# Kernel optimization log

Measured on AMD Instinct MI355X. Metric: run time of the kernel, lower is better.

Reference implementation:

```python
import jax, jax.numpy as jnp
import numpy as np

ALPHA = 0.2  # LeakyReLU negative slope
NEG_INF = -1e9


def setup_inputs() -> dict:
    key = jax.random.key(0)
    k1, k2, k3, k4 = jax.random.split(key, 4)
    B, N, Fin, Fout = 8, 2048, 128, 64
    h = jax.random.normal(k1, (B, N, Fin), dtype=jnp.float32)
    adj_mask = jax.random.randint(k2, (B, N, N), 0, 2).astype(jnp.int32)
    # xavier_uniform-style scales
    W = jax.random.uniform(k3, (Fout, Fin), dtype=jnp.float32,
                           minval=-1.0, maxval=1.0) * np.sqrt(6.0 / (Fin + Fout))
    a = jax.random.uniform(k4, (2 * Fout,), dtype=jnp.float32,
                           minval=-1.0, maxval=1.0) * np.sqrt(6.0 / (2 * Fout + 1))
    return {"h": h, "adj_mask": adj_mask, "W": W, "a": a}


def reference(h, adj_mask, W, a):
    # Wh: [B, N, Fout]
    Wh = jnp.einsum("bnf,of->bno", h, W)
    Fout = Wh.shape[-1]
    a1, a2 = a[:Fout], a[Fout:]
    # additive decomposition of a([Wh_i || Wh_j]): e_ij = leakyrelu(s1_i + s2_j)
    s1 = Wh @ a1  # [B, N]
    s2 = Wh @ a2  # [B, N]
    e = jax.nn.leaky_relu(s1[:, :, None] + s2[:, None, :], negative_slope=ALPHA)  # [B,N,N]
    e = jnp.where(adj_mask == 0, NEG_INF, e)
    attention = jax.nn.softmax(e, axis=-1)
    # dropout is identity in eval mode / p effectively 0 for the reference
    h_prime = jnp.einsum("bij,bjo->bio", attention, Wh)
    return h_prime
```

## Files before the change

kernel.cpp:

```cpp
#include <hip/hip_runtime.h>
#include <hip/hip_fp16.h>
#include <math.h>

#define LRELU_ALPHA 0.2f
#define NEG_INF -1000000000.0f

constexpr int B_ = 8, N_ = 2048, FIN = 128, FOUT = 64;

typedef _Float16 __attribute__((ext_vector_type(8))) f16x8;
typedef float __attribute__((ext_vector_type(4))) f32x4;

__device__ __forceinline__ void gload16(const void* g, void* l) {
  __builtin_amdgcn_global_load_lds(
      (const __attribute__((address_space(1))) void*)g,
      (__attribute__((address_space(3))) void*)l, 16, 0, 0);
}

__global__ __launch_bounds__(256) void k_wh(
    const float* __restrict__ h, const float* __restrict__ W,
    const float* __restrict__ a, unsigned short* __restrict__ WhT,
    float* __restrict__ s1, float* __restrict__ s2) {
  __shared__ float Wt[128][65];
  __shared__ float hs[16][128];

  const int t = threadIdx.x;
  const int row0 = blockIdx.x * 16;

  for (int e = t; e < 64 * 128; e += 256) {
    int o = e >> 7, f = e & 127;
    Wt[f][o] = W[e];
  }
  {
    const float4* hg = (const float4*)(h + (size_t)row0 * FIN);
    for (int i4 = t; i4 < 16 * 32; i4 += 256) {
      int r = i4 >> 5, f4 = i4 & 31;
      *(float4*)&hs[r][f4 * 4] = hg[i4];
    }
  }
  __syncthreads();

  const int wave = t >> 6, lane = t & 63;
  float acc[4] = {0.f, 0.f, 0.f, 0.f};
#pragma unroll 4
  for (int f4 = 0; f4 < 32; ++f4) {
    float w0 = Wt[4 * f4 + 0][lane], w1 = Wt[4 * f4 + 1][lane];
    float w2 = Wt[4 * f4 + 2][lane], w3 = Wt[4 * f4 + 3][lane];
#pragma unroll
    for (int r = 0; r < 4; ++r) {
      float4 hv = *(const float4*)&hs[wave * 4 + r][f4 * 4];
      acc[r] += hv.x * w0 + hv.y * w1 + hv.z * w2 + hv.w * w3;
    }
  }

  const float a1v = a[lane], a2v = a[64 + lane];
  const int b = row0 / N_;
#pragma unroll
  for (int r = 0; r < 4; ++r) {
    const int row = row0 + wave * 4 + r;
    const int n = row - b * N_;
    const float v = acc[r];
    WhT[((size_t)b * 64 + lane) * N_ + n] = __half_as_ushort(__float2half(v));
    float p1 = v * a1v, p2 = v * a2v;
#pragma unroll
    for (int d = 32; d; d >>= 1) {
      p1 += __shfl_xor(p1, d, 64);
      p2 += __shfl_xor(p2, d, 64);
    }
    if (lane == 0) { s1[row] = p1; s2[row] = p2; }
  }
}

__global__ __launch_bounds__(256, 2) void k_attn(
    const unsigned short* __restrict__ WhT,
    const float* __restrict__ s1g, const float* __restrict__ s2g,
    const int* __restrict__ adj, float* __restrict__ out) {
  __shared__ __align__(16) unsigned char sA[16 * 1024];
  __shared__ __align__(16) unsigned char sB[16 * 1024];
  __shared__ float s2s[N_];
  __shared__ float lsum_lds[32];

  const int t = threadIdx.x;
  const int wave = t >> 6, lane = t & 63;
  const int m = lane & 15, q = lane >> 4;
  const int b = blockIdx.y;
  const int i0 = blockIdx.x * 32;
  const int rg = wave & 1;
  const int p0 = (wave >> 1) * 2;

  const int* adjB = adj + (size_t)b * N_ * N_;
  const unsigned short* whB = WhT + (size_t)b * 64 * N_;
  const float* s2R = s2g + b * N_;

  for (int i = t; i < N_ / 4; i += 256)
    ((float4*)s2s)[i] = ((const float4*)s2R)[i];

  const float s1r = s1g[b * N_ + i0 + rg * 16 + m];

  const unsigned char* gp[4];
  int gstr;
  if (wave < 2) {
    const size_t r = (size_t)(i0 + wave * 16 + m);
#pragma unroll
    for (int ii = 0; ii < 4; ++ii) {
      int ks = ii >> 1, hh = ii & 1;
      gp[ii] = (const unsigned char*)(adjB + r * N_ + ks * 32 + q * 8 + hh * 4);
    }
    gstr = 64 * 4;
  } else {
#pragma unroll
    for (int ii = 0; ii < 4; ++ii) {
      int g = (wave - 2) * 2 + (ii >> 1), ks = ii & 1;
      gp[ii] = (const unsigned char*)(whB + (size_t)(g * 16 + m) * N_ +
                                      ks * 32 + q * 8);
    }
    gstr = 64 * 2;
  }

#define STAGE(S, c)                                                       \
  {                                                                       \
    _Pragma("unroll") for (int ii = 0; ii < 4; ++ii)                      \
        gload16(gp[ii] + (size_t)(c) * gstr, (S) + (wave * 4 + ii) * 1024); \
  }

  f32x4 acc0 = {0.f, 0.f, 0.f, 0.f}, acc1 = acc0;
  float lsum = 0.f;

  auto consume = [&](const unsigned char* base, int c) {
#pragma unroll
    for (int ks = 0; ks < 2; ++ks) {
      int4 A0 = *(const int4*)(base + (rg * 4 + ks * 2 + 0) * 1024 + lane * 16);
      int4 A1 = *(const int4*)(base + (rg * 4 + ks * 2 + 1) * 1024 + lane * 16);
      const float* sp = &s2s[c * 64 + ks * 32 + q * 8];
      float4 sv0 = *(const float4*)sp;
      float4 sv1 = *(const float4*)(sp + 4);
      float xs[8] = {sv0.x, sv0.y, sv0.z, sv0.w, sv1.x, sv1.y, sv1.z, sv1.w};
      int avs[8] = {A0.x, A0.y, A0.z, A0.w, A1.x, A1.y, A1.z, A1.w};
      f16x8 af;
#pragma unroll
      for (int j = 0; j < 8; ++j) {
        float x = s1r + xs[j];
        float e = fmaxf(x, LRELU_ALPHA * x);
        e = avs[j] ? (e - 2.0f) : NEG_INF;
        float p = __expf(e);
        lsum += p;
        af[j] = (_Float16)p;
      }
      f16x8 b0 = *(const f16x8*)(base + (8 + (p0 + 0) * 2 + ks) * 1024 + lane * 16);
      f16x8 b1 = *(const f16x8*)(base + (8 + (p0 + 1) * 2 + ks) * 1024 + lane * 16);
      acc0 = __builtin_amdgcn_mfma_f32_16x16x32_f16(af, b0, acc0, 0, 0, 0);
      acc1 = __builtin_amdgcn_mfma_f32_16x16x32_f16(af, b1, acc1, 0, 0, 0);
    }
  };

  STAGE(sA, 0);
  __syncthreads();

  for (int cc = 0; cc < 16; ++cc) {
    const int c0 = 2 * cc, c1 = 2 * cc + 1;
    STAGE(sB, c1);
    consume(sA, c0);
    __syncthreads();
    if (c1 + 1 < 32) STAGE(sA, c1 + 1);
    consume(sB, c1);
    __syncthreads();
  }

  lsum += __shfl_xor(lsum, 16, 64);
  lsum += __shfl_xor(lsum, 32, 64);
  if (wave < 2 && lane < 16) lsum_lds[wave * 16 + lane] = lsum;
  __syncthreads();

#pragma unroll
  for (int r = 0; r < 4; ++r) {
    const int ri = q * 4 + r;
    float l = lsum_lds[rg * 16 + ri];
    float inv = (l == 0.f) ? 1.f : 1.f / l;
    const size_t row = (size_t)b * N_ + i0 + rg * 16 + ri;
    out[row * FOUT + (p0 + 0) * 16 + m] = acc0[r] * inv;
    out[row * FOUT + (p0 + 1) * 16 + m] = acc1[r] * inv;
  }
#undef STAGE
}

extern "C" void kernel_launch(void* const* d_in, const int* in_sizes, int n_in,
                              void* d_out, int out_size, void* d_ws, size_t ws_size,
                              hipStream_t stream) {
  const float* h   = (const float*)d_in[0];
  const int*   adj = (const int*)d_in[1];
  const float* W   = (const float*)d_in[2];
  const float* a   = (const float*)d_in[3];
  float* out = (float*)d_out;

  unsigned short* WhT = (unsigned short*)d_ws;
  float* s1 = (float*)(WhT + (size_t)B_ * 64 * N_);
  float* s2 = s1 + (size_t)B_ * N_;

  k_wh<<<dim3(B_ * N_ / 16), 256, 0, stream>>>(h, W, a, WhT, s1, s2);
  k_attn<<<dim3(N_ / 32, B_), 256, 0, stream>>>(WhT, s1, s2, adj, out);
}
```

Baseline: 226.2 us.

## Split attention work over key dimension across waves with 16-row blocks

Each block now handles 16 query rows instead of 32. The four waves split the key chunk in half (jh) and the output columns in half (oh), and partial accumulators and row sums are reduced through LDS in the epilogue. Shared buffers shrink to 12 KB per stage and launch bounds go from 2 to 4 blocks per CU, doubling the grid to raise occupancy and latency hiding. In exchange, each block reloads the whole WhT stream for only 16 rows, which doubles Wh traffic per output row, and the epilogue adds an extra LDS reduction.

```diff
diff --git a/kernel.cpp b/kernel.cpp
--- a/kernel.cpp
+++ b/kernel.cpp
@@ -70,86 +70,83 @@
   }
 }
 
-__global__ __launch_bounds__(256, 2) void k_attn(
+__global__ __launch_bounds__(256, 4) void k_attn(
     const unsigned short* __restrict__ WhT,
     const float* __restrict__ s1g, const float* __restrict__ s2g,
     const int* __restrict__ adj, float* __restrict__ out) {
-  __shared__ __align__(16) unsigned char sA[16 * 1024];
-  __shared__ __align__(16) unsigned char sB[16 * 1024];
+  __shared__ __align__(16) unsigned char sA[12 * 1024];
+  __shared__ __align__(16) unsigned char sB[12 * 1024];
   __shared__ float s2s[N_];
-  __shared__ float lsum_lds[32];
 
   const int t = threadIdx.x;
   const int wave = t >> 6, lane = t & 63;
   const int m = lane & 15, q = lane >> 4;
   const int b = blockIdx.y;
-  const int i0 = blockIdx.x * 32;
-  const int rg = wave & 1;
-  const int p0 = (wave >> 1) * 2;
+  const int i0 = blockIdx.x * 16;
+  const int oh = wave & 1;
+  const int jh = wave >> 1;
 
   const int* adjB = adj + (size_t)b * N_ * N_;
   const unsigned short* whB = WhT + (size_t)b * 64 * N_;
-  const float* s2R = s2g + b * N_;
-
-  for (int i = t; i < N_ / 4; i += 256)
-    ((float4*)s2s)[i] = ((const float4*)s2R)[i];
-
-  const float s1r = s1g[b * N_ + i0 + rg * 16 + m];
-
-  const unsigned char* gp[4];
-  int gstr;
-  if (wave < 2) {
-    const size_t r = (size_t)(i0 + wave * 16 + m);
-#pragma unroll
-    for (int ii = 0; ii < 4; ++ii) {
+
+  {
+    const float4* s2R = (const float4*)(s2g + b * N_);
+    ((float4*)s2s)[t] = s2R[t];
+    ((float4*)s2s)[256 + t] = s2R[256 + t];
+  }
+
+  const float s1r = s1g[b * N_ + i0 + m];
+
+  const unsigned char* gp[3];
+  int gstr[3], loff[3];
+#pragma unroll
+  for (int k = 0; k < 3; ++k) {
+    const int ii = wave * 3 + k;
+    if (ii < 4) {
       int ks = ii >> 1, hh = ii & 1;
-      gp[ii] = (const unsigned char*)(adjB + r * N_ + ks * 32 + q * 8 + hh * 4);
-    }
-    gstr = 64 * 4;
-  } else {
-#pragma unroll
-    for (int ii = 0; ii < 4; ++ii) {
-      int g = (wave - 2) * 2 + (ii >> 1), ks = ii & 1;
-      gp[ii] = (const unsigned char*)(whB + (size_t)(g * 16 + m) * N_ +
-                                      ks * 32 + q * 8);
-    }
-    gstr = 64 * 2;
-  }
-
-#define STAGE(S, c)                                                       \
-  {                                                                       \
-    _Pragma("unroll") for (int ii = 0; ii < 4; ++ii)                      \
-        gload16(gp[ii] + (size_t)(c) * gstr, (S) + (wave * 4 + ii) * 1024); \
+      gp[k] = (const unsigned char*)(adjB + (size_t)(i0 + m) * N_ + ks * 32 +
+                                     q * 8 + hh * 4);
+      gstr[k] = 64 * 4;
+    } else {
+      int g = (ii - 4) >> 1, ks = (ii - 4) & 1;
+      gp[k] = (const unsigned char*)(whB + (size_t)(g * 16 + m) * N_ +
+                                     ks * 32 + q * 8);
+      gstr[k] = 64 * 2;
+    }
+    loff[k] = ii * 1024;
+  }
+
+#define STAGE(S, c)                                                      \
+  {                                                                      \
+    _Pragma("unroll") for (int k = 0; k < 3; ++k)                        \
+        gload16(gp[k] + (size_t)(c) * gstr[k], (S) + loff[k]);           \
   }
 
   f32x4 acc0 = {0.f, 0.f, 0.f, 0.f}, acc1 = acc0;
   float lsum = 0.f;
 
   auto consume = [&](const unsigned char* base, int c) {
-#pragma unroll
-    for (int ks = 0; ks < 2; ++ks) {
-      int4 A0 = *(const int4*)(base + (rg * 4 + ks * 2 + 0) * 1024 + lane * 16);
-      int4 A1 = *(const int4*)(base + (rg * 4 + ks * 2 + 1) * 1024 + lane * 16);
-      const float* sp = &s2s[c * 64 + ks * 32 + q * 8];
-      float4 sv0 = *(const float4*)sp;
-      float4 sv1 = *(const float4*)(sp + 4);
-      float xs[8] = {sv0.x, sv0.y, sv0.z, sv0.w, sv1.x, sv1.y, sv1.z, sv1.w};
-      int avs[8] = {A0.x, A0.y, A0.z, A0.w, A1.x, A1.y, A1.z, A1.w};
-      f16x8 af;
-#pragma unroll
-      for (int j = 0; j < 8; ++j) {
-        float x = s1r + xs[j];
-        float e = fmaxf(x, LRELU_ALPHA * x);
-        e = avs[j] ? (e - 2.0f) : NEG_INF;
-        float p = __expf(e);
-        lsum += p;
-        af[j] = (_Float16)p;
-      }
-      f16x8 b0 = *(const f16x8*)(base + (8 + (p0 + 0) * 2 + ks) * 1024 + lane * 16);
-      f16x8 b1 = *(const f16x8*)(base + (8 + (p0 + 1) * 2 + ks) * 1024 + lane * 16);
-      acc0 = __builtin_amdgcn_mfma_f32_16x16x32_f16(af, b0, acc0, 0, 0, 0);
-      acc1 = __builtin_amdgcn_mfma_f32_16x16x32_f16(af, b1, acc1, 0, 0, 0);
-    }
+    int4 A0 = *(const int4*)(base + (jh * 2 + 0) * 1024 + lane * 16);
+    int4 A1 = *(const int4*)(base + (jh * 2 + 1) * 1024 + lane * 16);
+    const float* sp = &s2s[c * 64 + jh * 32 + q * 8];
+    float4 sv0 = *(const float4*)sp;
+    float4 sv1 = *(const float4*)(sp + 4);
+    float xs[8] = {sv0.x, sv0.y, sv0.z, sv0.w, sv1.x, sv1.y, sv1.z, sv1.w};
+    int avs[8] = {A0.x, A0.y, A0.z, A0.w, A1.x, A1.y, A1.z, A1.w};
+    f16x8 af;
+#pragma unroll
+    for (int j = 0; j < 8; ++j) {
+      float x = s1r + xs[j];
+      float e = fmaxf(x, LRELU_ALPHA * x);
+      e = avs[j] ? (e - 2.0f) : NEG_INF;
+      float p = __expf(e);
+      lsum += p;
+      af[j] = (_Float16)p;
+    }
+    f16x8 b0 = *(const f16x8*)(base + (4 + (2 * oh) * 2 + jh) * 1024 + lane * 16);
+    f16x8 b1 = *(const f16x8*)(base + (4 + (2 * oh + 1) * 2 + jh) * 1024 + lane * 16);
+    acc0 = __builtin_amdgcn_mfma_f32_16x16x32_f16(af, b0, acc0, 0, 0, 0);
+    acc1 = __builtin_amdgcn_mfma_f32_16x16x32_f16(af, b1, acc1, 0, 0, 0);
   };
 
   STAGE(sA, 0);
@@ -165,19 +162,31 @@
     __syncthreads();
   }
 
+  float* accm = (float*)sA;
+  float* lsml = (float*)(sA + 8192);
+
   lsum += __shfl_xor(lsum, 16, 64);
   lsum += __shfl_xor(lsum, 32, 64);
-  if (wave < 2 && lane < 16) lsum_lds[wave * 16 + lane] = lsum;
+  if (lane < 16) lsml[wave * 16 + lane] = lsum;
+#pragma unroll
+  for (int r = 0; r < 4; ++r) {
+    accm[(wave * 64 + lane) * 8 + r] = acc0[r];
+    accm[(wave * 64 + lane) * 8 + 4 + r] = acc1[r];
+  }
   __syncthreads();
 
 #pragma unroll
-  for (int r = 0; r < 4; ++r) {
-    const int ri = q * 4 + r;
-    float l = lsum_lds[rg * 16 + ri];
-    float inv = (l == 0.f) ? 1.f : 1.f / l;
-    const size_t row = (size_t)b * N_ + i0 + rg * 16 + ri;
-    out[row * FOUT + (p0 + 0) * 16 + m] = acc0[r] * inv;
-    out[row * FOUT + (p0 + 1) * 16 + m] = acc1[r] * inv;
+  for (int kk = 0; kk < 4; ++kk) {
+    int e = kk * 256 + t;
+    int ri = e >> 6, o = e & 63;
+    int og = o >> 4, ohp = og >> 1, a = og & 1;
+    int sl = (ri >> 2) * 16 + (o & 15);
+    int slot = a * 4 + (ri & 3);
+    float v = accm[(ohp * 64 + sl) * 8 + slot] +
+              accm[((2 + ohp) * 64 + sl) * 8 + slot];
+    float l = lsml[ri] + lsml[2 * 16 + ri];
+    if (l == 0.f) l = 1.f;
+    out[((size_t)b * N_ + i0 + ri) * FOUT + o] = v / l;
   }
 #undef STAGE
 }
@@ -196,5 +205,5 @@
   float* s2 = s1 + (size_t)B_ * N_;
 
   k_wh<<<dim3(B_ * N_ / 16), 256, 0, stream>>>(h, W, a, WhT, s1, s2);
-  k_attn<<<dim3(N_ / 32, B_), 256, 0, stream>>>(WhT, s1, s2, adj, out);
-}
+  k_attn<<<dim3(N_ / 16, B_), 256, 0, stream>>>(WhT, s1, s2, adj, out);
+}
```

Result: slower. 232.2 us (+2.6%).

## Pack adjacency mask into bitmask before attention kernel

Applied to the files above, without the earlier changes.

Adds a pre-pass kernel that compresses the int32 adjacency mask into one bit per entry. The attention kernel then loads each row's mask words into registers up front and shares them across lanes with shuffles, so its LDS double-buffer carries only the fp16 Wh tiles. Each stage now covers 128 columns with all four waves loading Wh, and the row-sum reduction uses shuffles instead of LDS plus a barrier. The full mask is still read once, now in a separate streaming kernel with an extra launch, in exchange for a lighter, less latency-bound main loop.

```diff
diff --git a/kernel.cpp b/kernel.cpp
--- a/kernel.cpp
+++ b/kernel.cpp
@@ -14,6 +14,24 @@
   __builtin_amdgcn_global_load_lds(
       (const __attribute__((address_space(1))) void*)g,
       (__attribute__((address_space(3))) void*)l, 16, 0, 0);
+}
+
+__global__ __launch_bounds__(256) void k_pack(const int* __restrict__ adj,
+                                              unsigned int* __restrict__ bits) {
+  const size_t g = (size_t)blockIdx.x * 256 + threadIdx.x;
+  const int4* src = (const int4*)adj + g * 8;
+  int4 v[8];
+#pragma unroll
+  for (int c = 0; c < 8; ++c) v[c] = src[c];
+  unsigned int w = 0;
+#pragma unroll
+  for (int c = 0; c < 8; ++c) {
+    w |= (v[c].x != 0 ? 1u : 0u) << (c * 4 + 0);
+    w |= (v[c].y != 0 ? 1u : 0u) << (c * 4 + 1);
+    w |= (v[c].z != 0 ? 1u : 0u) << (c * 4 + 2);
+    w |= (v[c].w != 0 ? 1u : 0u) << (c * 4 + 3);
+  }
+  bits[g] = w;
 }
 
 __global__ __launch_bounds__(256) void k_wh(
@@ -73,11 +91,10 @@
 __global__ __launch_bounds__(256, 2) void k_attn(
     const unsigned short* __restrict__ WhT,
     const float* __restrict__ s1g, const float* __restrict__ s2g,
-    const int* __restrict__ adj, float* __restrict__ out) {
+    const unsigned int* __restrict__ bits, float* __restrict__ out) {
   __shared__ __align__(16) unsigned char sA[16 * 1024];
   __shared__ __align__(16) unsigned char sB[16 * 1024];
   __shared__ float s2s[N_];
-  __shared__ float lsum_lds[32];
 
   const int t = threadIdx.x;
   const int wave = t >> 6, lane = t & 63;
@@ -85,68 +102,59 @@
   const int b = blockIdx.y;
   const int i0 = blockIdx.x * 32;
   const int rg = wave & 1;
-  const int p0 = (wave >> 1) * 2;
-
-  const int* adjB = adj + (size_t)b * N_ * N_;
+  const int oh = wave >> 1;
+
   const unsigned short* whB = WhT + (size_t)b * 64 * N_;
-  const float* s2R = s2g + b * N_;
-
-  for (int i = t; i < N_ / 4; i += 256)
-    ((float4*)s2s)[i] = ((const float4*)s2R)[i];
+
+  {
+    const float4* s2R = (const float4*)(s2g + b * N_);
+    ((float4*)s2s)[t] = s2R[t];
+    ((float4*)s2s)[256 + t] = s2R[256 + t];
+  }
 
   const float s1r = s1g[b * N_ + i0 + rg * 16 + m];
 
+  const unsigned int* bitsrow =
+      bits + ((size_t)b * N_ + i0 + rg * 16 + m) * (N_ / 32);
+  unsigned int bw[16];
+#pragma unroll
+  for (int c = 0; c < 16; ++c) bw[c] = bitsrow[c * 4 + q];
+
   const unsigned char* gp[4];
-  int gstr;
-  if (wave < 2) {
-    const size_t r = (size_t)(i0 + wave * 16 + m);
-#pragma unroll
-    for (int ii = 0; ii < 4; ++ii) {
-      int ks = ii >> 1, hh = ii & 1;
-      gp[ii] = (const unsigned char*)(adjB + r * N_ + ks * 32 + q * 8 + hh * 4);
-    }
-    gstr = 64 * 4;
-  } else {
-#pragma unroll
-    for (int ii = 0; ii < 4; ++ii) {
-      int g = (wave - 2) * 2 + (ii >> 1), ks = ii & 1;
-      gp[ii] = (const unsigned char*)(whB + (size_t)(g * 16 + m) * N_ +
-                                      ks * 32 + q * 8);
-    }
-    gstr = 64 * 2;
-  }
-
-#define STAGE(S, c)                                                       \
-  {                                                                       \
-    _Pragma("unroll") for (int ii = 0; ii < 4; ++ii)                      \
-        gload16(gp[ii] + (size_t)(c) * gstr, (S) + (wave * 4 + ii) * 1024); \
+#pragma unroll
+  for (int ks = 0; ks < 4; ++ks)
+    gp[ks] = (const unsigned char*)(whB + (size_t)(wave * 16 + m) * N_ +
+                                    ks * 32 + q * 8);
+
+#define STAGE(S, c)                                                     \
+  {                                                                     \
+    _Pragma("unroll") for (int ks = 0; ks < 4; ++ks)                    \
+        gload16(gp[ks] + (size_t)(c) * 256, (S) + (wave * 4 + ks) * 1024); \
   }
 
   f32x4 acc0 = {0.f, 0.f, 0.f, 0.f}, acc1 = acc0;
   float lsum = 0.f;
 
-  auto consume = [&](const unsigned char* base, int c) {
-#pragma unroll
-    for (int ks = 0; ks < 2; ++ks) {
-      int4 A0 = *(const int4*)(base + (rg * 4 + ks * 2 + 0) * 1024 + lane * 16);
-      int4 A1 = *(const int4*)(base + (rg * 4 + ks * 2 + 1) * 1024 + lane * 16);
-      const float* sp = &s2s[c * 64 + ks * 32 + q * 8];
+  auto consume = [&](const unsigned char* base, unsigned int word, int c) {
+#pragma unroll
+    for (int ks = 0; ks < 4; ++ks) {
+      unsigned int ws = __shfl((int)word, ks * 16 + m, 64);
+      const float* sp = &s2s[c * 128 + ks * 32 + q * 8];
       float4 sv0 = *(const float4*)sp;
       float4 sv1 = *(const float4*)(sp + 4);
       float xs[8] = {sv0.x, sv0.y, sv0.z, sv0.w, sv1.x, sv1.y, sv1.z, sv1.w};
-      int avs[8] = {A0.x, A0.y, A0.z, A0.w, A1.x, A1.y, A1.z, A1.w};
       f16x8 af;
 #pragma unroll
       for (int j = 0; j < 8; ++j) {
         float x = s1r + xs[j];
         float e = fmaxf(x, LRELU_ALPHA * x);
-        e = avs[j] ? (e - 2.0f) : NEG_INF;
+        e = ((ws >> (q * 8 + j)) & 1u) ? (e - 2.0f) : NEG_INF;
         float p = __expf(e);
         lsum += p;
         af[j] = (_Float16)p;
       }
-      f16x8 b0 = *(const f16x8*)(base + (8 + (p0 + 0) * 2 + ks) * 1024 + lane * 16);
-      f16x8 b1 = *(const f16x8*)(base + (8 + (p0 + 1) * 2 + ks) * 1024 + lane * 16);
+      f16x8 b0 = *(const f16x8*)(base + ((2 * oh + 0) * 4 + ks) * 1024 + lane * 16);
+      f16x8 b1 = *(const f16x8*)(base + ((2 * oh + 1) * 4 + ks) * 1024 + lane * 16);
       acc0 = __builtin_amdgcn_mfma_f32_16x16x32_f16(af, b0, acc0, 0, 0, 0);
       acc1 = __builtin_amdgcn_mfma_f32_16x16x32_f16(af, b1, acc1, 0, 0, 0);
     }
@@ -155,29 +163,28 @@
   STAGE(sA, 0);
   __syncthreads();
 
-  for (int cc = 0; cc < 16; ++cc) {
+#pragma unroll
+  for (int cc = 0; cc < 8; ++cc) {
     const int c0 = 2 * cc, c1 = 2 * cc + 1;
     STAGE(sB, c1);
-    consume(sA, c0);
+    consume(sA, bw[c0], c0);
     __syncthreads();
-    if (c1 + 1 < 32) STAGE(sA, c1 + 1);
-    consume(sB, c1);
+    if (c1 + 1 < 16) STAGE(sA, c1 + 1);
+    consume(sB, bw[c1], c1);
     __syncthreads();
   }
 
   lsum += __shfl_xor(lsum, 16, 64);
   lsum += __shfl_xor(lsum, 32, 64);
-  if (wave < 2 && lane < 16) lsum_lds[wave * 16 + lane] = lsum;
-  __syncthreads();
 
 #pragma unroll
   for (int r = 0; r < 4; ++r) {
     const int ri = q * 4 + r;
-    float l = lsum_lds[rg * 16 + ri];
+    float l = __shfl(lsum, ri, 64);
     float inv = (l == 0.f) ? 1.f : 1.f / l;
     const size_t row = (size_t)b * N_ + i0 + rg * 16 + ri;
-    out[row * FOUT + (p0 + 0) * 16 + m] = acc0[r] * inv;
-    out[row * FOUT + (p0 + 1) * 16 + m] = acc1[r] * inv;
+    out[row * FOUT + (2 * oh + 0) * 16 + m] = acc0[r] * inv;
+    out[row * FOUT + (2 * oh + 1) * 16 + m] = acc1[r] * inv;
   }
 #undef STAGE
 }
@@ -194,7 +201,10 @@
   unsigned short* WhT = (unsigned short*)d_ws;
   float* s1 = (float*)(WhT + (size_t)B_ * 64 * N_);
   float* s2 = s1 + (size_t)B_ * N_;
-
+  unsigned int* bits = (unsigned int*)(s2 + (size_t)B_ * N_);
+
+  const int nwords = B_ * N_ * (N_ / 32);
+  k_pack<<<dim3(nwords / 256), 256, 0, stream>>>(adj, bits);
   k_wh<<<dim3(B_ * N_ / 16), 256, 0, stream>>>(h, W, a, WhT, s1, s2);
-  k_attn<<<dim3(N_ / 32, B_), 256, 0, stream>>>(WhT, s1, s2, adj, out);
-}
+  k_attn<<<dim3(N_ / 32, B_), 256, 0, stream>>>(WhT, s1, s2, bits, out);
+}
```

Result: slower. 321.3 us (+42.1%).
